# Performance work log

Hardware: AMD Instinct MI355X
Metric: run time of the kernel (lower is better)

The kernel has to match this reference:

```python
import jax, jax.numpy as jnp
from jax import lax
import numpy as np

B, TE, TD, C, H, L, V, BLOCK = 2, 1024, 1024, 512, 8, 4, 32000, 1024
HD = C // H  # 64


def setup_inputs() -> dict:
    key = jax.random.key(0)
    ks = iter(jax.random.split(key, 64))
    def w(*shape):
        return jax.random.normal(next(ks), shape, jnp.float32) * 0.02
    d = {}
    d["enc_inp"] = jax.random.randint(next(ks), (B, TE), 0, V, dtype=jnp.int32)
    d["dec_inp"] = jax.random.randint(next(ks), (B, TD), 0, V, dtype=jnp.int32)
    d["enc_inp_mask"] = jnp.ones((B, TE), jnp.int32)
    d["tok_emb"] = w(V, C)
    d["pos_emb"] = w(BLOCK, C)
    for p in ["e", "d_sa", "d_ca"]:
        d[p + "_wq"] = w(L, H, C, HD)
        d[p + "_wk"] = w(L, H, C, HD)
        d[p + "_wv"] = w(L, H, C, HD)
        d[p + "_wo"] = w(L, C, C)
        d[p + "_bo"] = jnp.zeros((L, C), jnp.float32)
    for n in ["e_ln1", "e_ln2", "d_ln1", "d_ln2", "d_ln3"]:
        d[n + "_g"] = jnp.ones((L, C), jnp.float32)
        d[n + "_b"] = jnp.zeros((L, C), jnp.float32)
    for p in ["e", "d"]:
        d[p + "_w1"] = w(L, C, 4 * C)
        d[p + "_b1"] = jnp.zeros((L, 4 * C), jnp.float32)
        d[p + "_w2"] = w(L, 4 * C, C)
        d[p + "_b2"] = jnp.zeros((L, C), jnp.float32)
    d["out_w"] = w(C, V)
    d["out_b"] = jnp.zeros((V,), jnp.float32)
    return d


def _ln(x, g, b):
    m = jnp.mean(x, -1, keepdims=True)
    v = jnp.mean((x - m) ** 2, -1, keepdims=True)
    return (x - m) / jnp.sqrt(v + 1e-5) * g + b


def _mha(x, kv, wq, wk, wv, wo, bo, mask, causal):
    # x: [B,T,C], kv: [B,S,C], wq/wk/wv: [H,C,HD]
    q = jnp.einsum('btc,hcd->bhtd', x, wq)
    k = jnp.einsum('bsc,hcd->bhsd', kv, wk)
    v = jnp.einsum('bsc,hcd->bhsd', kv, wv)
    s = jnp.einsum('bhtd,bhsd->bhts', q, k) * (HD ** -0.5)
    if causal:
        T, S = s.shape[-2], s.shape[-1]
        s = jnp.where(jnp.tril(jnp.ones((T, S), bool)), s, -jnp.inf)
    if mask is not None:
        s = jnp.where(mask[:, None, None, :] != 0, s, -jnp.inf)
    a = jax.nn.softmax(s, axis=-1)
    o = jnp.einsum('bhts,bhsd->bthd', a, v).reshape(x.shape[0], x.shape[1], -1)
    return o @ wo + bo


def reference(enc_inp, dec_inp, enc_inp_mask, tok_emb, pos_emb,
              e_wq, e_wk, e_wv, e_wo, e_bo,
              d_sa_wq, d_sa_wk, d_sa_wv, d_sa_wo, d_sa_bo,
              d_ca_wq, d_ca_wk, d_ca_wv, d_ca_wo, d_ca_bo,
              e_ln1_g, e_ln1_b, e_ln2_g, e_ln2_b,
              d_ln1_g, d_ln1_b, d_ln2_g, d_ln2_b, d_ln3_g, d_ln3_b,
              e_w1, e_b1, e_w2, e_b2, d_w1, d_b1, d_w2, d_b2,
              out_w, out_b):
    enc = tok_emb[enc_inp] + pos_emb[:enc_inp.shape[1]]
    dec = tok_emb[dec_inp] + pos_emb[:dec_inp.shape[1]]

    def enc_step(x, p):
        ln1g, ln1b, wq, wk, wv, wo, bo, ln2g, ln2b, w1, b1, w2, b2 = p
        h = _ln(x, ln1g, ln1b)
        x = x + _mha(h, h, wq, wk, wv, wo, bo, enc_inp_mask, False)
        h = _ln(x, ln2g, ln2b)
        x = x + jnp.maximum(h @ w1 + b1, 0.0) @ w2 + b2
        return x, None

    enc_out, _ = lax.scan(enc_step, enc, (e_ln1_g, e_ln1_b, e_wq, e_wk, e_wv, e_wo, e_bo,
                                          e_ln2_g, e_ln2_b, e_w1, e_b1, e_w2, e_b2))

    def dec_step(x, p):
        (ln1g, ln1b, sawq, sawk, sawv, sawo, sabo,
         ln2g, ln2b, cawq, cawk, cawv, cawo, cabo,
         ln3g, ln3b, w1, b1, w2, b2) = p
        h = _ln(x, ln1g, ln1b)
        x = x + _mha(h, h, sawq, sawk, sawv, sawo, sabo, None, True)
        # torch code applies the same cross-attn LayerNorm to both x and encoder_output
        hq = _ln(x, ln2g, ln2b)
        hk = _ln(enc_out, ln2g, ln2b)
        x = x + _mha(hq, hk, cawq, cawk, cawv, cawo, cabo, enc_inp_mask, False)
        h = _ln(x, ln3g, ln3b)
        x = x + jnp.maximum(h @ w1 + b1, 0.0) @ w2 + b2
        return x, None

    dec_out, _ = lax.scan(dec_step, dec, (d_ln1_g, d_ln1_b, d_sa_wq, d_sa_wk, d_sa_wv, d_sa_wo, d_sa_bo,
                                          d_ln2_g, d_ln2_b, d_ca_wq, d_ca_wk, d_ca_wv, d_ca_wo, d_ca_bo,
                                          d_ln3_g, d_ln3_b, d_w1, d_b1, d_w2, d_b2))

    logits = dec_out @ out_w + out_b  # [B, T_dec, V]
    return logits
```

## Files before the change

### kernel.cpp

```cpp
#include <hip/hip_runtime.h>
#include <hip/hip_bf16.h>
#include <math.h>

#define Cdim 512
#define Hn   8
#define HDim 64
#define Ld   4
#define Tn   1024
#define Bn   2
#define NTOK 2048
#define FF   2048
#define Vn   32000

typedef __bf16 bf16_t;
typedef __bf16 bf16x8 __attribute__((ext_vector_type(8)));
typedef __bf16 bf16x4 __attribute__((ext_vector_type(4)));
typedef float  f32x4  __attribute__((ext_vector_type(4)));

__device__ __forceinline__ void ln_wave(const float* __restrict__ xr,
    const float* __restrict__ g, const float* __restrict__ bb,
    bf16_t* __restrict__ yr, int lane)
{
    f32x4 a = *(const f32x4*)&xr[lane * 8];
    f32x4 c = *(const f32x4*)&xr[lane * 8 + 4];
    float s = a[0] + a[1] + a[2] + a[3] + c[0] + c[1] + c[2] + c[3];
    #pragma unroll
    for (int o = 1; o < 64; o <<= 1) s += __shfl_xor(s, o, 64);
    float mean = s * (1.f / Cdim);
    float d[8], qv = 0.f;
    #pragma unroll
    for (int k = 0; k < 4; k++) { d[k] = a[k] - mean; d[4 + k] = c[k] - mean; }
    #pragma unroll
    for (int k = 0; k < 8; k++) qv += d[k] * d[k];
    #pragma unroll
    for (int o = 1; o < 64; o <<= 1) qv += __shfl_xor(qv, o, 64);
    float inv = rsqrtf(qv * (1.f / Cdim) + 1e-5f);
    f32x4 g0 = *(const f32x4*)&g[lane * 8],  g1 = *(const f32x4*)&g[lane * 8 + 4];
    f32x4 b0 = *(const f32x4*)&bb[lane * 8], b1 = *(const f32x4*)&bb[lane * 8 + 4];
    bf16x8 o;
    #pragma unroll
    for (int k = 0; k < 4; k++) {
        o[k]     = (bf16_t)(d[k]     * inv * g0[k] + b0[k]);
        o[4 + k] = (bf16_t)(d[4 + k] * inv * g1[k] + b1[k]);
    }
    *(bf16x8*)&yr[lane * 8] = o;
}

__global__ __launch_bounds__(256) void ln_k(const float* __restrict__ x,
    const float* __restrict__ g, const float* __restrict__ bb, bf16_t* __restrict__ y)
{
    int wid = threadIdx.x >> 6, lane = threadIdx.x & 63;
    int row = blockIdx.x * 4 + wid;
    ln_wave(x + (long)row * Cdim, g, bb, y + (long)row * Cdim, lane);
}

__global__ __launch_bounds__(256) void ln2_k(const float* __restrict__ x1,
    const float* __restrict__ x2, const float* __restrict__ g,
    const float* __restrict__ bb, bf16_t* __restrict__ y1, bf16_t* __restrict__ y2)
{
    int wid = threadIdx.x >> 6, lane = threadIdx.x & 63;
    int row = blockIdx.x * 4 + wid;
    const float* x = (row < NTOK) ? x1 : x2;
    bf16_t*      y = (row < NTOK) ? y1 : y2;
    int r = row & (NTOK - 1);
    ln_wave(x + (long)r * Cdim, g, bb, y + (long)r * Cdim, lane);
}

__global__ __launch_bounds__(256) void embed_ln_k(const int* __restrict__ inp,
    const float* __restrict__ tok, const float* __restrict__ pos,
    const float* __restrict__ g, const float* __restrict__ bb,
    float* __restrict__ x, bf16_t* __restrict__ y)
{
    int wid = threadIdx.x >> 6, lane = threadIdx.x & 63;
    int bt = blockIdx.x * 4 + wid;
    int t = bt & (Tn - 1);
    long toff = (long)inp[bt] * Cdim;
    f32x4 a = *(const f32x4*)&tok[toff + lane * 8];
    f32x4 c = *(const f32x4*)&tok[toff + lane * 8 + 4];
    f32x4 pa = *(const f32x4*)&pos[(long)t * Cdim + lane * 8];
    f32x4 pc = *(const f32x4*)&pos[(long)t * Cdim + lane * 8 + 4];
    a += pa; c += pc;
    float* xr = x + (long)bt * Cdim;
    *(f32x4*)&xr[lane * 8] = a;
    *(f32x4*)&xr[lane * 8 + 4] = c;
    float s = a[0] + a[1] + a[2] + a[3] + c[0] + c[1] + c[2] + c[3];
    #pragma unroll
    for (int o = 1; o < 64; o <<= 1) s += __shfl_xor(s, o, 64);
    float mean = s * (1.f / Cdim);
    float d[8], qv = 0.f;
    #pragma unroll
    for (int k = 0; k < 4; k++) { d[k] = a[k] - mean; d[4 + k] = c[k] - mean; }
    #pragma unroll
    for (int k = 0; k < 8; k++) qv += d[k] * d[k];
    #pragma unroll
    for (int o = 1; o < 64; o <<= 1) qv += __shfl_xor(qv, o, 64);
    float inv = rsqrtf(qv * (1.f / Cdim) + 1e-5f);
    f32x4 g0 = *(const f32x4*)&g[lane * 8],  g1 = *(const f32x4*)&g[lane * 8 + 4];
    f32x4 b0 = *(const f32x4*)&bb[lane * 8], b1 = *(const f32x4*)&bb[lane * 8 + 4];
    bf16x8 o;
    #pragma unroll
    for (int k = 0; k < 4; k++) {
        o[k]     = (bf16_t)(d[k]     * inv * g0[k] + b0[k]);
        o[4 + k] = (bf16_t)(d[4 + k] * inv * g1[k] + b1[k]);
    }
    *(bf16x8*)&y[(long)bt * Cdim + lane * 8] = o;
}

struct Ptr3 { const float* p[3]; };
__global__ __launch_bounds__(256) void tcvt_b_k(Ptr3 srcs, bf16_t* __restrict__ dst,
    int R, int Cc, int lps, long dstStride)
{
    int z = blockIdx.z; int s = z / lps, l = z - s * lps;
    const float* in = srcs.p[s] + (long)l * R * Cc;
    bf16_t* op = dst + (long)z * dstStride;
    __shared__ float t[64][65];
    int r0 = blockIdx.y * 64, c0 = blockIdx.x * 64;
    int tx = threadIdx.x & 63, ty = threadIdx.x >> 6;
    #pragma unroll
    for (int i = 0; i < 16; i++)
        t[ty + i * 4][tx] = in[(long)(r0 + ty + i * 4) * Cc + c0 + tx];
    __syncthreads();
    #pragma unroll
    for (int i = 0; i < 16; i++) {
        int cc = ty + i * 4;
        op[(long)(c0 + cc) * R + r0 + tx] = (bf16_t)t[tx][cc];
    }
}

struct QkvSrc { const float* p[9]; };
__global__ __launch_bounds__(256) void tcvt_qkv_k(QkvSrc srcs, bf16_t* __restrict__ outp)
{
    int z = blockIdx.z;
    int si = z >> 5, zb = (z >> 3) & 3, zh = z & 7;
    int set = si / 3, part = si - set * 3;
    const float* in = srcs.p[si] + (long)zb * (Hn * Cdim * HDim) + (long)zh * (Cdim * HDim);
    bf16_t* op = outp + ((long)set * Ld + zb) * (1536L * Cdim)
                      + (long)part * 512 * Cdim + (long)zh * 64 * Cdim;
    __shared__ float t[64][65];
    int r0 = blockIdx.y * 64;
    int tx = threadIdx.x & 63, ty = threadIdx.x >> 6;
    #pragma unroll
    for (int i = 0; i < 16; i++)
        t[ty + i * 4][tx] = in[(long)(r0 + ty + i * 4) * HDim + tx];
    __syncthreads();
    #pragma unroll
    for (int i = 0; i < 16; i++) {
        int cc = ty + i * 4;
        op[(long)cc * Cdim + r0 + tx] = (bf16_t)t[tx][cc];
    }
}

template<int BM, int BN, int BK, bool BIAS, bool RELU, bool RES, bool OBF,
         bool VOUT, int SWZM, bool XOUT, bool COAL>
__global__ __launch_bounds__(256) void mgemm_k(
    const bf16_t* __restrict__ A, const bf16_t* __restrict__ A2, int aSplit,
    const bf16_t* __restrict__ Bt, const float* __restrict__ bias,
    const float* __restrict__ res, void* __restrict__ Cout,
    bf16_t* __restrict__ xout, bf16_t* __restrict__ vtout, int vSplit,
    int K, int lda, int ldb, int ldc)
{
    constexpr int MR = BM / 32;
    constexpr int NR = BN / 32;
    constexpr int KK = BK / 32;
    constexpr int LPR = BK / 8;
    __shared__ bf16_t As0[BM * BK];
    __shared__ bf16_t As1[BM * BK];
    __shared__ bf16_t Bs0[BN * BK];
    __shared__ bf16_t Bs1[BN * BK];
    __shared__ float cws[COAL ? 4 * 16 * 36 : 1];

    int tid = threadIdx.x;
    int wv = tid >> 6, lane = tid & 63;
    int bm, bn;
    if constexpr (SWZM > 0) {
        int lin = blockIdx.y * gridDim.x + blockIdx.x;
        int tot = gridDim.x * gridDim.y;
        int chunk = tot >> 3;
        int e = (lin & 7) * chunk + (lin >> 3);
        bm = (e % SWZM) * BM;
        bn = (e / SWZM) * BN;
    } else {
        bm = blockIdx.y * BM; bn = blockIdx.x * BN;
    }
    const bf16_t* Ab = (bn < aSplit) ? A : A2;
    int wr = wv >> 1, wc = wv & 1;

    f32x4 acc[MR][NR];
    #pragma unroll
    for (int i = 0; i < MR; i++)
        #pragma unroll
        for (int j = 0; j < NR; j++)
            acc[i][j] = (f32x4){0.f, 0.f, 0.f, 0.f};

    constexpr int RPW = 512 / BK;
    constexpr int RPP = 2048 / BK;
    const int sr  = lane / LPR;
    const int sc8 = ((lane % LPR) ^ (sr & (LPR - 1))) * 8;
    const int r16 = lane & 15, g4 = lane >> 4;

    auto stage = [&](int k0, bf16_t (&Asb)[BM * BK], bf16_t (&Bsb)[BN * BK]) {
        #pragma unroll
        for (int p = 0; p < BM * BK / 2048; p++) {
            int rb = p * RPP + wv * RPW;
            const bf16_t* g = Ab + (long)(bm + rb + sr) * lda + (k0 + sc8);
            __builtin_amdgcn_global_load_lds(
                (const __attribute__((address_space(1))) void*)g,
                (__attribute__((address_space(3))) void*)&Asb[rb * BK],
                16, 0, 0);
        }
        #pragma unroll
        for (int p = 0; p < BN * BK / 2048; p++) {
            int rb = p * RPP + wv * RPW;
            const bf16_t* g = Bt + (long)(bn + rb + sr) * ldb + (k0 + sc8);
            __builtin_amdgcn_global_load_lds(
                (const __attribute__((address_space(1))) void*)g,
                (__attribute__((address_space(3))) void*)&Bsb[rb * BK],
                16, 0, 0);
        }
    };
    auto compute = [&](bf16_t (&Asb)[BM * BK], bf16_t (&Bsb)[BN * BK]) {
        #pragma unroll
        for (int kk = 0; kk < KK; kk++) {
            bf16x8 bkk[NR];
            #pragma unroll
            for (int j = 0; j < NR; j++) {
                int row = wc * (BN / 2) + j * 16 + r16;
                bkk[j] = *(const bf16x8*)&Bsb[row * BK + (((kk * 4 + g4) ^ (row & (LPR - 1))) * 8)];
            }
            #pragma unroll
            for (int i = 0; i < MR; i++) {
                int row = wr * (BM / 2) + i * 16 + r16;
                bf16x8 a = *(const bf16x8*)&Asb[row * BK + (((kk * 4 + g4) ^ (row & (LPR - 1))) * 8)];
                #pragma unroll
                for (int j = 0; j < NR; j++)
                    acc[i][j] = __builtin_amdgcn_mfma_f32_16x16x32_bf16(a, bkk[j], acc[i][j], 0, 0, 0);
            }
        }
    };

    int nIt = K / BK;
    stage(0, As0, Bs0);
    for (int it = 0; it < nIt; it += 2) {
        __syncthreads();
        if (it + 1 < nIt) stage((it + 1) * BK, As1, Bs1);
        compute(As0, Bs0);
        __syncthreads();
        if (it + 2 < nIt) stage((it + 2) * BK, As0, Bs0);
        if (it + 1 < nIt) compute(As1, Bs1);
    }

    if constexpr (COAL) {
        #pragma unroll
        for (int i = 0; i < MR; i++) {
            int gr0 = bm + wr * (BM / 2) + i * 16;
            #pragma unroll
            for (int hh = 0; hh < NR / 2; hh++) {
                #pragma unroll
                for (int jj = 0; jj < 2; jj++) {
                    int j = hh * 2 + jj;
                    int gc = bn + wc * (BN / 2) + j * 16 + r16;
                    float bv = BIAS ? bias[gc] : 0.f;
                    #pragma unroll
                    for (int q = 0; q < 4; q++) {
                        float v = acc[i][j][q];
                        if (BIAS) v += bv;
                        if (RELU) v = fmaxf(v, 0.f);
                        cws[(wv * 16 + g4 * 4 + q) * 36 + jj * 16 + r16] = v;
                    }
                }
                int gcb = bn + wc * (BN / 2) + hh * 32;
                if constexpr (OBF) {
                    int row = lane >> 2, c8 = (lane & 3) * 8;
                    f32x4 v0 = *(f32x4*)&cws[(wv * 16 + row) * 36 + c8];
                    f32x4 v1 = *(f32x4*)&cws[(wv * 16 + row) * 36 + c8 + 4];
                    long oidx = (long)(gr0 + row) * ldc + gcb + c8;
                    bf16x8 o;
                    #pragma unroll
                    for (int k = 0; k < 4; k++) { o[k] = (bf16_t)v0[k]; o[4 + k] = (bf16_t)v1[k]; }
                    *(bf16x8*)&((bf16_t*)Cout)[oidx] = o;
                } else {
                    #pragma unroll
                    for (int ps = 0; ps < 2; ps++) {
                        int row = (lane >> 3) + 8 * ps, c4 = (lane & 7) * 4;
                        f32x4 v = *(f32x4*)&cws[(wv * 16 + row) * 36 + c4];
                        long oidx = (long)(gr0 + row) * ldc + gcb + c4;
                        if (RES) v += *(const f32x4*)&res[oidx];
                        *(f32x4*)&((float*)Cout)[oidx] = v;
                        if (XOUT) {
                            bf16x4 o;
                            #pragma unroll
                            for (int k = 0; k < 4; k++) o[k] = (bf16_t)v[k];
                            *(bf16x4*)&xout[oidx] = o;
                        }
                    }
                }
            }
        }
    } else {
        #pragma unroll
        for (int i = 0; i < MR; i++) {
            #pragma unroll
            for (int j = 0; j < NR; j++) {
                int gr = bm + wr * (BM / 2) + i * 16 + g4 * 4;
                int gc = bn + wc * (BN / 2) + j * 16 + r16;
                float bv = BIAS ? bias[gc] : 0.f;
                #pragma unroll
                for (int q = 0; q < 4; q++) {
                    float v = acc[i][j][q];
                    if (BIAS) v += bv;
                    if (RELU) v = fmaxf(v, 0.f);
                    if (VOUT && gc >= vSplit) {
                        int row = gr + q;
                        int b = row >> 10, t = row & (Tn - 1);
                        vtout[((long)b * 512 + (gc - vSplit)) * Tn + t] = (bf16_t)v;
                    } else {
                        long oidx = (long)(gr + q) * ldc + gc;
                        if (RES)  v += res[oidx];
                        if (OBF) ((bf16_t*)Cout)[oidx] = (bf16_t)v;
                        else     ((float*) Cout)[oidx] = v;
                        if (XOUT) xout[oidx] = (bf16_t)v;
                    }
                }
            }
        }
    }
}

template<bool CAUSAL, bool HASMASK>
__global__ __launch_bounds__(512, 2) void flash_k(
    const bf16_t* __restrict__ qkv, const bf16_t* __restrict__ vt,
    const int* __restrict__ mask, bf16_t* __restrict__ ao)
{
    __shared__ bf16_t Kl[2][2][64][72];
    __shared__ bf16_t Vl[2][2][64][72];
    __shared__ bf16_t Pl[8][16][72];

    int qt = blockIdx.x, bh = blockIdx.y;
    int b = bh >> 3, h = bh & 7;
    int tid = threadIdx.x, wv = tid >> 6, lane = tid & 63;
    int wg = wv >> 2, wq4 = wv & 3;
    int r16 = lane & 15, g4 = lane >> 4;
    int gtid = tid & 255;

    const bf16_t* qb = qkv + ((long)(b * Tn + qt * 64 + wq4 * 16 + r16)) * 1536 + h * 64;
    bf16x8 aq0 = *(const bf16x8*)&qb[g4 * 8];
    bf16x8 aq1 = *(const bf16x8*)&qb[32 + g4 * 8];

    f32x4 acc[4];
    #pragma unroll
    for (int j = 0; j < 4; j++) acc[j] = (f32x4){0.f, 0.f, 0.f, 0.f};
    float m_[4], l_[4];
    #pragma unroll
    for (int q = 0; q < 4; q++) { m_[q] = -1e30f; l_[q] = 0.f; }

    int lastT = CAUSAL ? qt : (Tn / 64 - 1);
    int niter = CAUSAL ? (qt / 2 + 1) : (Tn / 128);
    int krow = gtid >> 3, kcol = (gtid & 7) * 8;

    bf16x8 kr[2], vr[2];
    int mv = 0;
    {
        int t0 = wg;
        if (t0 <= lastT) {
            int s0 = t0 * 64;
            #pragma unroll
            for (int i = 0; i < 2; i++)
                kr[i] = *(const bf16x8*)&qkv[((long)(b * Tn + s0 + krow + i * 32)) * 1536 + 512 + h * 64 + kcol];
            #pragma unroll
            for (int i = 0; i < 2; i++)
                vr[i] = *(const bf16x8*)&vt[((long)(bh * 64 + krow + i * 32)) * Tn + s0 + kcol];
            if (HASMASK) mv = mask[b * Tn + s0 + lane];
        }
    }

    for (int it = 0; it < niter; it++) {
        int cur = it & 1;
        int t = 2 * it + wg;
        bool active = t <= lastT;
        if (active) {
            #pragma unroll
            for (int i = 0; i < 2; i++) *(bf16x8*)&Kl[cur][wg][krow + i * 32][kcol] = kr[i];
            #pragma unroll
            for (int i = 0; i < 2; i++) *(bf16x8*)&Vl[cur][wg][krow + i * 32][kcol] = vr[i];
        }
        int mv_use = mv;
        __syncthreads();
        int tn = t + 2;
        if (it + 1 < niter && tn <= lastT) {
            int sn = tn * 64;
            #pragma unroll
            for (int i = 0; i < 2; i++)
                kr[i] = *(const bf16x8*)&qkv[((long)(b * Tn + sn + krow + i * 32)) * 1536 + 512 + h * 64 + kcol];
            #pragma unroll
            for (int i = 0; i < 2; i++)
                vr[i] = *(const bf16x8*)&vt[((long)(bh * 64 + krow + i * 32)) * Tn + sn + kcol];
            if (HASMASK) mv = mask[b * Tn + sn + lane];
        }
        if (!active) continue;

        f32x4 scv[4];
        __builtin_amdgcn_s_setprio(1);
        #pragma unroll
        for (int j = 0; j < 4; j++) {
            scv[j] = (f32x4){0.f, 0.f, 0.f, 0.f};
            bf16x8 bk0 = *(const bf16x8*)&Kl[cur][wg][j * 16 + r16][g4 * 8];
            bf16x8 bk1 = *(const bf16x8*)&Kl[cur][wg][j * 16 + r16][32 + g4 * 8];
            scv[j] = __builtin_amdgcn_mfma_f32_16x16x32_bf16(aq0, bk0, scv[j], 0, 0, 0);
            scv[j] = __builtin_amdgcn_mfma_f32_16x16x32_bf16(aq1, bk1, scv[j], 0, 0, 0);
        }
        __builtin_amdgcn_s_setprio(0);

        bool diag = CAUSAL && (t == qt);
        #pragma unroll
        for (int j = 0; j < 4; j++) {
            int col = j * 16 + r16;
            int mm = 1;
            if (HASMASK) mm = __shfl(mv_use, col, 64);
            #pragma unroll
            for (int q = 0; q < 4; q++) {
                float v = scv[j][q] * 0.125f;
                if (diag && col > wq4 * 16 + g4 * 4 + q) v = -1e30f;
                if (HASMASK && mm == 0) v = -1e30f;
                scv[j][q] = v;
            }
        }

        float pmax[4];
        #pragma unroll
        for (int q = 0; q < 4; q++) {
            float v = fmaxf(fmaxf(scv[0][q], scv[1][q]), fmaxf(scv[2][q], scv[3][q]));
            v = fmaxf(v, __shfl_xor(v, 1, 64));
            v = fmaxf(v, __shfl_xor(v, 2, 64));
            v = fmaxf(v, __shfl_xor(v, 4, 64));
            v = fmaxf(v, __shfl_xor(v, 8, 64));
            pmax[q] = v;
        }
        bool skip = __all(pmax[0] <= m_[0] + 8.f && pmax[1] <= m_[1] + 8.f &&
                          pmax[2] <= m_[2] + 8.f && pmax[3] <= m_[3] + 8.f);
        if (!skip) {
            #pragma unroll
            for (int q = 0; q < 4; q++) {
                float mnew = fmaxf(m_[q], pmax[q]);
                float rf = __expf(m_[q] - mnew);
                l_[q] *= rf;
                #pragma unroll
                for (int j = 0; j < 4; j++) acc[j][q] *= rf;
                m_[q] = mnew;
            }
        }
        #pragma unroll
        for (int q = 0; q < 4; q++) {
            float rs = 0.f;
            #pragma unroll
            for (int j = 0; j < 4; j++) {
                float pv = __expf(scv[j][q] - m_[q]);
                scv[j][q] = pv;
                rs += pv;
            }
            rs += __shfl_xor(rs, 1, 64);
            rs += __shfl_xor(rs, 2, 64);
            rs += __shfl_xor(rs, 4, 64);
            rs += __shfl_xor(rs, 8, 64);
            l_[q] += rs;
        }

        #pragma unroll
        for (int j = 0; j < 4; j++)
            #pragma unroll
            for (int q = 0; q < 4; q++)
                Pl[wv][g4 * 4 + q][j * 16 + r16] = (bf16_t)scv[j][q];
        asm volatile("s_waitcnt lgkmcnt(0)" ::: "memory");
        __builtin_amdgcn_sched_barrier(0);

        __builtin_amdgcn_s_setprio(1);
        #pragma unroll
        for (int c = 0; c < 2; c++) {
            bf16x8 pa = *(const bf16x8*)&Pl[wv][r16][c * 32 + g4 * 8];
            #pragma unroll
            for (int j = 0; j < 4; j++) {
                bf16x8 bv = *(const bf16x8*)&Vl[cur][wg][j * 16 + r16][c * 32 + g4 * 8];
                acc[j] = __builtin_amdgcn_mfma_f32_16x16x32_bf16(pa, bv, acc[j], 0, 0, 0);
            }
        }
        __builtin_amdgcn_s_setprio(0);
    }

    float* accS = (float*)&Kl[0][0][0][0];
    float* mlS  = accS + 64 * 64;
    __syncthreads();
    if (wg == 1) {
        #pragma unroll
        for (int j = 0; j < 4; j++)
            #pragma unroll
            for (int q = 0; q < 4; q++)
                accS[(wq4 * 16 + g4 * 4 + q) * 64 + j * 16 + r16] = acc[j][q];
        if (r16 == 0)
            #pragma unroll
            for (int q = 0; q < 4; q++) {
                mlS[(wq4 * 16 + g4 * 4 + q) * 2 + 0] = m_[q];
                mlS[(wq4 * 16 + g4 * 4 + q) * 2 + 1] = l_[q];
            }
    }
    __syncthreads();
    if (wg == 0) {
        bf16_t* aob = ao + ((long)(b * Tn + qt * 64 + wq4 * 16 + g4 * 4)) * Cdim + h * 64;
        #pragma unroll
        for (int q = 0; q < 4; q++) {
            int row = wq4 * 16 + g4 * 4 + q;
            float mB = mlS[row * 2], lB = mlS[row * 2 + 1];
            float mS = fmaxf(m_[q], mB);
            float fA = __expf(m_[q] - mS), fB = __expf(mB - mS);
            float lS = l_[q] * fA + lB * fB;
            float inv = 1.f / lS;
            #pragma unroll
            for (int j = 0; j < 4; j++) {
                float o = (acc[j][q] * fA + accS[row * 64 + j * 16 + r16] * fB) * inv;
                aob[(long)q * Cdim + j * 16 + r16] = (bf16_t)o;
            }
        }
    }
}

static void run_attn(hipStream_t stream, const bf16_t* hq, const bf16_t* hkv,
    const bf16_t* wqkv, const float* bo, const bf16_t* wo_t,
    float* xres, const int* mask, bool causal,
    bf16_t* qkv, bf16_t* vt, bf16_t* ao)
{
    dim3 blk(256);
    mgemm_k<64,128,64,false,false,false,true,true,0,false,false><<<dim3(12, 32, 1), blk, 0, stream>>>(
        hq, hkv, 512, wqkv, nullptr, nullptr, qkv, nullptr, vt, 1024,
        Cdim, Cdim, Cdim, 1536);
    if (causal)
        flash_k<true,false><<<dim3(Tn / 64, Bn * Hn), dim3(512), 0, stream>>>(qkv, vt, nullptr, ao);
    else
        flash_k<false,true><<<dim3(Tn / 64, Bn * Hn), dim3(512), 0, stream>>>(qkv, vt, mask, ao);
    mgemm_k<64,64,64,true,false,true,false,false,0,false,true><<<dim3(8, 32, 1), blk, 0, stream>>>(
        ao, ao, 1 << 30, wo_t, bo, xres, xres, nullptr, nullptr, 1 << 30,
        Cdim, Cdim, Cdim, Cdim);
}

extern "C" void kernel_launch(void* const* d_in, const int* in_sizes, int n_in,
                              void* d_out, int out_size, void* d_ws, size_t ws_size,
                              hipStream_t stream)
{
    (void)in_sizes; (void)n_in; (void)out_size; (void)ws_size;
    const int*   enc_inp  = (const int*)d_in[0];
    const int*   dec_inp  = (const int*)d_in[1];
    const int*   enc_mask = (const int*)d_in[2];
    const float* tok_emb  = (const float*)d_in[3];
    const float* pos_emb  = (const float*)d_in[4];
    const float* e_wq  = (const float*)d_in[5];
    const float* e_wk  = (const float*)d_in[6];
    const float* e_wv  = (const float*)d_in[7];
    const float* e_wo  = (const float*)d_in[8];
    const float* e_bo  = (const float*)d_in[9];
    const float* dsa_wq = (const float*)d_in[10];
    const float* dsa_wk = (const float*)d_in[11];
    const float* dsa_wv = (const float*)d_in[12];
    const float* dsa_wo = (const float*)d_in[13];
    const float* dsa_bo = (const float*)d_in[14];
    const float* dca_wq = (const float*)d_in[15];
    const float* dca_wk = (const float*)d_in[16];
    const float* dca_wv = (const float*)d_in[17];
    const float* dca_wo = (const float*)d_in[18];
    const float* dca_bo = (const float*)d_in[19];
    const float* e_ln1_g = (const float*)d_in[20];
    const float* e_ln1_b = (const float*)d_in[21];
    const float* e_ln2_g = (const float*)d_in[22];
    const float* e_ln2_b = (const float*)d_in[23];
    const float* d_ln1_g = (const float*)d_in[24];
    const float* d_ln1_b = (const float*)d_in[25];
    const float* d_ln2_g = (const float*)d_in[26];
    const float* d_ln2_b = (const float*)d_in[27];
    const float* d_ln3_g = (const float*)d_in[28];
    const float* d_ln3_b = (const float*)d_in[29];
    const float* e_w1 = (const float*)d_in[30];
    const float* e_b1 = (const float*)d_in[31];
    const float* e_w2 = (const float*)d_in[32];
    const float* e_b2 = (const float*)d_in[33];
    const float* d_w1 = (const float*)d_in[34];
    const float* d_b1 = (const float*)d_in[35];
    const float* d_w2 = (const float*)d_in[36];
    const float* d_b2 = (const float*)d_in[37];
    const float* out_w = (const float*)d_in[38];
    const float* out_b = (const float*)d_in[39];
    float* out = (float*)d_out;

    char* p = (char*)d_ws;
    auto takeB = [&](size_t bytes) { char* r = p; p += (bytes + 255) & ~(size_t)255; return r; };
    float*  x_enc = (float*)takeB(1048576ull * 4);
    float*  x_dec = (float*)takeB(1048576ull * 4);
    bf16_t* h     = (bf16_t*)takeB(1048576ull * 2);
    bf16_t* hk    = (bf16_t*)takeB(1048576ull * 2);
    bf16_t* qkv   = (bf16_t*)takeB(3145728ull * 2);
    bf16_t* vt    = (bf16_t*)takeB(1048576ull * 2);
    bf16_t* ao    = (bf16_t*)takeB(1048576ull * 2);
    bf16_t* xdb   = (bf16_t*)takeB(1048576ull * 2);
    bf16_t* mid   = (bf16_t*)takeB(4194304ull * 2);
    bf16_t* wqkv_t = (bf16_t*)takeB(12ull * 786432 * 2);
    bf16_t* wo_t   = (bf16_t*)takeB(12ull * 262144 * 2);
    bf16_t* w1_t   = (bf16_t*)takeB(8ull * 1048576 * 2);
    bf16_t* w2_t   = (bf16_t*)takeB(8ull * 1048576 * 2);
    bf16_t* outw_t = (bf16_t*)takeB(16384000ull * 2);

    dim3 blk(256);
    const long LQKV = 1536L * Cdim;

    QkvSrc qs;
    qs.p[0] = e_wq;   qs.p[1] = e_wk;   qs.p[2] = e_wv;
    qs.p[3] = dsa_wq; qs.p[4] = dsa_wk; qs.p[5] = dsa_wv;
    qs.p[6] = dca_wq; qs.p[7] = dca_wk; qs.p[8] = dca_wv;
    tcvt_qkv_k<<<dim3(1, 8, 288), blk, 0, stream>>>(qs, wqkv_t);
    Ptr3 pw;
    pw.p[0] = e_wo; pw.p[1] = dsa_wo; pw.p[2] = dca_wo;
    tcvt_b_k<<<dim3(8, 8, 12), blk, 0, stream>>>(pw, wo_t, Cdim, Cdim, 4, (long)Cdim * Cdim);
    pw.p[0] = e_w1; pw.p[1] = d_w1; pw.p[2] = nullptr;
    tcvt_b_k<<<dim3(32, 8, 8), blk, 0, stream>>>(pw, w1_t, Cdim, FF, 4, (long)Cdim * FF);
    pw.p[0] = e_w2; pw.p[1] = d_w2; pw.p[2] = nullptr;
    tcvt_b_k<<<dim3(8, 32, 8), blk, 0, stream>>>(pw, w2_t, FF, Cdim, 4, (long)FF * Cdim);
    pw.p[0] = out_w; pw.p[1] = nullptr; pw.p[2] = nullptr;
    tcvt_b_k<<<dim3(500, 8, 1), blk, 0, stream>>>(pw, outw_t, Cdim, Vn, 1, 0);

    embed_ln_k<<<NTOK / 4, blk, 0, stream>>>(enc_inp, tok_emb, pos_emb, e_ln1_g, e_ln1_b, x_enc, h);
    for (int l = 0; l < Ld; l++) {
        if (l) ln_k<<<NTOK / 4, blk, 0, stream>>>(x_enc, e_ln1_g + l * Cdim, e_ln1_b + l * Cdim, h);
        run_attn(stream, h, h,
                 wqkv_t + (long)l * LQKV, e_bo + l * Cdim, wo_t + (long)l * Cdim * Cdim,
                 x_enc, enc_mask, false, qkv, vt, ao);
        ln_k<<<NTOK / 4, blk, 0, stream>>>(x_enc, e_ln2_g + l * Cdim, e_ln2_b + l * Cdim, h);
        mgemm_k<128,128,64,true,true,false,true,false,0,false,true><<<dim3(16, 16, 1), blk, 0, stream>>>(
            h, h, 1 << 30, w1_t + (long)l * Cdim * FF, e_b1 + l * FF, nullptr, mid,
            nullptr, nullptr, 1 << 30, Cdim, Cdim, Cdim, FF);
        mgemm_k<64,64,64,true,false,true,false,false,0,false,true><<<dim3(8, 32, 1), blk, 0, stream>>>(
            mid, mid, 1 << 30, w2_t + (long)l * FF * Cdim, e_b2 + l * Cdim, x_enc, x_enc,
            nullptr, nullptr, 1 << 30, FF, FF, FF, Cdim);
    }

    embed_ln_k<<<NTOK / 4, blk, 0, stream>>>(dec_inp, tok_emb, pos_emb, d_ln1_g, d_ln1_b, x_dec, h);
    for (int l = 0; l < Ld; l++) {
        if (l) ln_k<<<NTOK / 4, blk, 0, stream>>>(x_dec, d_ln1_g + l * Cdim, d_ln1_b + l * Cdim, h);
        run_attn(stream, h, h,
                 wqkv_t + (long)(Ld + l) * LQKV, dsa_bo + l * Cdim,
                 wo_t + (long)(Ld + l) * Cdim * Cdim,
                 x_dec, nullptr, true, qkv, vt, ao);
        ln2_k<<<2 * NTOK / 4, blk, 0, stream>>>(x_dec, x_enc,
            d_ln2_g + l * Cdim, d_ln2_b + l * Cdim, h, hk);
        run_attn(stream, h, hk,
                 wqkv_t + (long)(2 * Ld + l) * LQKV, dca_bo + l * Cdim,
                 wo_t + (long)(2 * Ld + l) * Cdim * Cdim,
                 x_dec, enc_mask, false, qkv, vt, ao);
        ln_k<<<NTOK / 4, blk, 0, stream>>>(x_dec, d_ln3_g + l * Cdim, d_ln3_b + l * Cdim, h);
        mgemm_k<128,128,64,true,true,false,true,false,0,false,true><<<dim3(16, 16, 1), blk, 0, stream>>>(
            h, h, 1 << 30, w1_t + (long)(Ld + l) * Cdim * FF, d_b1 + l * FF, nullptr, mid,
            nullptr, nullptr, 1 << 30, Cdim, Cdim, Cdim, FF);
        if (l < Ld - 1)
            mgemm_k<64,64,64,true,false,true,false,false,0,false,true><<<dim3(8, 32, 1), blk, 0, stream>>>(
                mid, mid, 1 << 30, w2_t + (long)(Ld + l) * FF * Cdim, d_b2 + l * Cdim, x_dec, x_dec,
                nullptr, nullptr, 1 << 30, FF, FF, FF, Cdim);
        else
            mgemm_k<64,64,64,true,false,true,false,false,0,true,true><<<dim3(8, 32, 1), blk, 0, stream>>>(
                mid, mid, 1 << 30, w2_t + (long)(Ld + l) * FF * Cdim, d_b2 + l * Cdim, x_dec, x_dec,
                xdb, nullptr, 1 << 30, FF, FF, FF, Cdim);
    }

    mgemm_k<128,128,64,true,false,false,false,false,16,false,true><<<dim3(250, 16, 1), blk, 0, stream>>>(
        xdb, xdb, 1 << 30, outw_t, out_b, nullptr, out, nullptr, nullptr, 1 << 30,
        Cdim, Cdim, Cdim, Vn);
}
```

Before: 1.005 ms.

## Shrink flash-attention blocks to 32 query rows with 4 waves, single-buffered LDS

The flash attention kernel now handles 32 query rows per block with 256 threads (two KV groups of two waves each) instead of 64 rows with 512 threads. This doubles the grid and spreads the causal workload more evenly across CUs. The K/V shared tiles drop from double to single buffering, with a second barrier per iteration to keep reuse safe. The smaller LDS footprint and the new launch bounds allow more blocks per CU, at the cost of an extra sync per iteration and re-loading K/V for each half of the former query tile.

```diff
diff --git a/kernel.cpp b/kernel.cpp
--- a/kernel.cpp
+++ b/kernel.cpp
@@ -327,22 +327,21 @@
 }
 
 template<bool CAUSAL, bool HASMASK>
-__global__ __launch_bounds__(512, 2) void flash_k(
+__global__ __launch_bounds__(256, 3) void flash_k(
     const bf16_t* __restrict__ qkv, const bf16_t* __restrict__ vt,
     const int* __restrict__ mask, bf16_t* __restrict__ ao)
 {
-    __shared__ bf16_t Kl[2][2][64][72];
-    __shared__ bf16_t Vl[2][2][64][72];
-    __shared__ bf16_t Pl[8][16][72];
-
-    int qt = blockIdx.x, bh = blockIdx.y;
+    __shared__ bf16_t Kl[2][64][72];
+    __shared__ bf16_t Vl[2][64][72];
+    __shared__ bf16_t Pl[4][16][72];
+
+    int qx = blockIdx.x, bh = blockIdx.y;
     int b = bh >> 3, h = bh & 7;
     int tid = threadIdx.x, wv = tid >> 6, lane = tid & 63;
-    int wg = wv >> 2, wq4 = wv & 3;
+    int wg = wv >> 1, wq = wv & 1;
     int r16 = lane & 15, g4 = lane >> 4;
-    int gtid = tid & 255;
-
-    const bf16_t* qb = qkv + ((long)(b * Tn + qt * 64 + wq4 * 16 + r16)) * 1536 + h * 64;
+
+    const bf16_t* qb = qkv + ((long)(b * Tn + qx * 32 + wq * 16 + r16)) * 1536 + h * 64;
     bf16x8 aq0 = *(const bf16x8*)&qb[g4 * 8];
     bf16x8 aq1 = *(const bf16x8*)&qb[32 + g4 * 8];
 
@@ -353,35 +352,35 @@
     #pragma unroll
     for (int q = 0; q < 4; q++) { m_[q] = -1e30f; l_[q] = 0.f; }
 
-    int lastT = CAUSAL ? qt : (Tn / 64 - 1);
-    int niter = CAUSAL ? (qt / 2 + 1) : (Tn / 128);
-    int krow = gtid >> 3, kcol = (gtid & 7) * 8;
-
-    bf16x8 kr[2], vr[2];
+    int lastT = CAUSAL ? (qx >> 1) : (Tn / 64 - 1);
+    int niter = CAUSAL ? ((qx >> 2) + 1) : (Tn / 128);
+    int st = tid & 127;
+    int srow = st >> 3, scol = (st & 7) * 8;
+
+    bf16x8 kr[4], vr[4];
     int mv = 0;
     {
         int t0 = wg;
         if (t0 <= lastT) {
             int s0 = t0 * 64;
             #pragma unroll
-            for (int i = 0; i < 2; i++)
-                kr[i] = *(const bf16x8*)&qkv[((long)(b * Tn + s0 + krow + i * 32)) * 1536 + 512 + h * 64 + kcol];
-            #pragma unroll
-            for (int i = 0; i < 2; i++)
-                vr[i] = *(const bf16x8*)&vt[((long)(bh * 64 + krow + i * 32)) * Tn + s0 + kcol];
+            for (int i = 0; i < 4; i++)
+                kr[i] = *(const bf16x8*)&qkv[((long)(b * Tn + s0 + srow + i * 16)) * 1536 + 512 + h * 64 + scol];
+            #pragma unroll
+            for (int i = 0; i < 4; i++)
+                vr[i] = *(const bf16x8*)&vt[((long)(bh * 64 + srow + i * 16)) * Tn + s0 + scol];
             if (HASMASK) mv = mask[b * Tn + s0 + lane];
         }
     }
 
     for (int it = 0; it < niter; it++) {
-        int cur = it & 1;
         int t = 2 * it + wg;
         bool active = t <= lastT;
         if (active) {
             #pragma unroll
-            for (int i = 0; i < 2; i++) *(bf16x8*)&Kl[cur][wg][krow + i * 32][kcol] = kr[i];
-            #pragma unroll
-            for (int i = 0; i < 2; i++) *(bf16x8*)&Vl[cur][wg][krow + i * 32][kcol] = vr[i];
+            for (int i = 0; i < 4; i++) *(bf16x8*)&Kl[wg][srow + i * 16][scol] = kr[i];
+            #pragma unroll
+            for (int i = 0; i < 4; i++) *(bf16x8*)&Vl[wg][srow + i * 16][scol] = vr[i];
         }
         int mv_use = mv;
         __syncthreads();
@@ -389,124 +388,124 @@
         if (it + 1 < niter && tn <= lastT) {
             int sn = tn * 64;
             #pragma unroll
-            for (int i = 0; i < 2; i++)
-                kr[i] = *(const bf16x8*)&qkv[((long)(b * Tn + sn + krow + i * 32)) * 1536 + 512 + h * 64 + kcol];
-            #pragma unroll
-            for (int i = 0; i < 2; i++)
-                vr[i] = *(const bf16x8*)&vt[((long)(bh * 64 + krow + i * 32)) * Tn + sn + kcol];
+            for (int i = 0; i < 4; i++)
+                kr[i] = *(const bf16x8*)&qkv[((long)(b * Tn + sn + srow + i * 16)) * 1536 + 512 + h * 64 + scol];
+            #pragma unroll
+            for (int i = 0; i < 4; i++)
+                vr[i] = *(const bf16x8*)&vt[((long)(bh * 64 + srow + i * 16)) * Tn + sn + scol];
             if (HASMASK) mv = mask[b * Tn + sn + lane];
         }
-        if (!active) continue;
-
-        f32x4 scv[4];
-        __builtin_amdgcn_s_setprio(1);
-        #pragma unroll
-        for (int j = 0; j < 4; j++) {
-            scv[j] = (f32x4){0.f, 0.f, 0.f, 0.f};
-            bf16x8 bk0 = *(const bf16x8*)&Kl[cur][wg][j * 16 + r16][g4 * 8];
-            bf16x8 bk1 = *(const bf16x8*)&Kl[cur][wg][j * 16 + r16][32 + g4 * 8];
-            scv[j] = __builtin_amdgcn_mfma_f32_16x16x32_bf16(aq0, bk0, scv[j], 0, 0, 0);
-            scv[j] = __builtin_amdgcn_mfma_f32_16x16x32_bf16(aq1, bk1, scv[j], 0, 0, 0);
-        }
-        __builtin_amdgcn_s_setprio(0);
-
-        bool diag = CAUSAL && (t == qt);
-        #pragma unroll
-        for (int j = 0; j < 4; j++) {
-            int col = j * 16 + r16;
-            int mm = 1;
-            if (HASMASK) mm = __shfl(mv_use, col, 64);
+        if (active) {
+            f32x4 scv[4];
+            __builtin_amdgcn_s_setprio(1);
+            #pragma unroll
+            for (int j = 0; j < 4; j++) {
+                scv[j] = (f32x4){0.f, 0.f, 0.f, 0.f};
+                bf16x8 bk0 = *(const bf16x8*)&Kl[wg][j * 16 + r16][g4 * 8];
+                bf16x8 bk1 = *(const bf16x8*)&Kl[wg][j * 16 + r16][32 + g4 * 8];
+                scv[j] = __builtin_amdgcn_mfma_f32_16x16x32_bf16(aq0, bk0, scv[j], 0, 0, 0);
+                scv[j] = __builtin_amdgcn_mfma_f32_16x16x32_bf16(aq1, bk1, scv[j], 0, 0, 0);
+            }
+            __builtin_amdgcn_s_setprio(0);
+
+            bool diag = CAUSAL && (t == lastT);
+            #pragma unroll
+            for (int j = 0; j < 4; j++) {
+                int col = j * 16 + r16;
+                int mm = 1;
+                if (HASMASK) mm = __shfl(mv_use, col, 64);
+                #pragma unroll
+                for (int q = 0; q < 4; q++) {
+                    float v = scv[j][q] * 0.125f;
+                    if (diag && col > (qx & 1) * 32 + wq * 16 + g4 * 4 + q) v = -1e30f;
+                    if (HASMASK && mm == 0) v = -1e30f;
+                    scv[j][q] = v;
+                }
+            }
+
+            float pmax[4];
             #pragma unroll
             for (int q = 0; q < 4; q++) {
-                float v = scv[j][q] * 0.125f;
-                if (diag && col > wq4 * 16 + g4 * 4 + q) v = -1e30f;
-                if (HASMASK && mm == 0) v = -1e30f;
-                scv[j][q] = v;
-            }
-        }
-
-        float pmax[4];
-        #pragma unroll
-        for (int q = 0; q < 4; q++) {
-            float v = fmaxf(fmaxf(scv[0][q], scv[1][q]), fmaxf(scv[2][q], scv[3][q]));
-            v = fmaxf(v, __shfl_xor(v, 1, 64));
-            v = fmaxf(v, __shfl_xor(v, 2, 64));
-            v = fmaxf(v, __shfl_xor(v, 4, 64));
-            v = fmaxf(v, __shfl_xor(v, 8, 64));
-            pmax[q] = v;
-        }
-        bool skip = __all(pmax[0] <= m_[0] + 8.f && pmax[1] <= m_[1] + 8.f &&
-                          pmax[2] <= m_[2] + 8.f && pmax[3] <= m_[3] + 8.f);
-        if (!skip) {
+                float v = fmaxf(fmaxf(scv[0][q], scv[1][q]), fmaxf(scv[2][q], scv[3][q]));
+                v = fmaxf(v, __shfl_xor(v, 1, 64));
+                v = fmaxf(v, __shfl_xor(v, 2, 64));
+                v = fmaxf(v, __shfl_xor(v, 4, 64));
+                v = fmaxf(v, __shfl_xor(v, 8, 64));
+                pmax[q] = v;
+            }
+            bool skip = __all(pmax[0] <= m_[0] + 8.f && pmax[1] <= m_[1] + 8.f &&
+                              pmax[2] <= m_[2] + 8.f && pmax[3] <= m_[3] + 8.f);
+            if (!skip) {
+                #pragma unroll
+                for (int q = 0; q < 4; q++) {
+                    float mnew = fmaxf(m_[q], pmax[q]);
+                    float rf = __expf(m_[q] - mnew);
+                    l_[q] *= rf;
+                    #pragma unroll
+                    for (int j = 0; j < 4; j++) acc[j][q] *= rf;
+                    m_[q] = mnew;
+                }
+            }
             #pragma unroll
             for (int q = 0; q < 4; q++) {
-                float mnew = fmaxf(m_[q], pmax[q]);
-                float rf = __expf(m_[q] - mnew);
-                l_[q] *= rf;
-                #pragma unroll
-                for (int j = 0; j < 4; j++) acc[j][q] *= rf;
-                m_[q] = mnew;
-            }
-        }
-        #pragma unroll
-        for (int q = 0; q < 4; q++) {
-            float rs = 0.f;
-            #pragma unroll
-            for (int j = 0; j < 4; j++) {
-                float pv = __expf(scv[j][q] - m_[q]);
-                scv[j][q] = pv;
-                rs += pv;
-            }
-            rs += __shfl_xor(rs, 1, 64);
-            rs += __shfl_xor(rs, 2, 64);
-            rs += __shfl_xor(rs, 4, 64);
-            rs += __shfl_xor(rs, 8, 64);
-            l_[q] += rs;
-        }
-
+                float rs = 0.f;
+                #pragma unroll
+                for (int j = 0; j < 4; j++) {
+                    float pv = __expf(scv[j][q] - m_[q]);
+                    scv[j][q] = pv;
+                    rs += pv;
+                }
+                rs += __shfl_xor(rs, 1, 64);
+                rs += __shfl_xor(rs, 2, 64);
+                rs += __shfl_xor(rs, 4, 64);
+                rs += __shfl_xor(rs, 8, 64);
+                l_[q] += rs;
+            }
+
+            #pragma unroll
+            for (int j = 0; j < 4; j++)
+                #pragma unroll
+                for (int q = 0; q < 4; q++)
+                    Pl[wv][g4 * 4 + q][j * 16 + r16] = (bf16_t)scv[j][q];
+            asm volatile("s_waitcnt lgkmcnt(0)" ::: "memory");
+            __builtin_amdgcn_sched_barrier(0);
+
+            __builtin_amdgcn_s_setprio(1);
+            #pragma unroll
+            for (int c = 0; c < 2; c++) {
+                bf16x8 pa = *(const bf16x8*)&Pl[wv][r16][c * 32 + g4 * 8];
+                #pragma unroll
+                for (int j = 0; j < 4; j++) {
+                    bf16x8 bv = *(const bf16x8*)&Vl[wg][j * 16 + r16][c * 32 + g4 * 8];
+                    acc[j] = __builtin_amdgcn_mfma_f32_16x16x32_bf16(pa, bv, acc[j], 0, 0, 0);
+                }
+            }
+            __builtin_amdgcn_s_setprio(0);
+        }
+        __syncthreads();
+    }
+
+    float* accS = (float*)&Kl[0][0][0];
+    float* mlS  = accS + 32 * 64;
+    if (wg == 1) {
         #pragma unroll
         for (int j = 0; j < 4; j++)
             #pragma unroll
             for (int q = 0; q < 4; q++)
-                Pl[wv][g4 * 4 + q][j * 16 + r16] = (bf16_t)scv[j][q];
-        asm volatile("s_waitcnt lgkmcnt(0)" ::: "memory");
-        __builtin_amdgcn_sched_barrier(0);
-
-        __builtin_amdgcn_s_setprio(1);
-        #pragma unroll
-        for (int c = 0; c < 2; c++) {
-            bf16x8 pa = *(const bf16x8*)&Pl[wv][r16][c * 32 + g4 * 8];
-            #pragma unroll
-            for (int j = 0; j < 4; j++) {
-                bf16x8 bv = *(const bf16x8*)&Vl[cur][wg][j * 16 + r16][c * 32 + g4 * 8];
-                acc[j] = __builtin_amdgcn_mfma_f32_16x16x32_bf16(pa, bv, acc[j], 0, 0, 0);
-            }
-        }
-        __builtin_amdgcn_s_setprio(0);
-    }
-
-    float* accS = (float*)&Kl[0][0][0][0];
-    float* mlS  = accS + 64 * 64;
-    __syncthreads();
-    if (wg == 1) {
-        #pragma unroll
-        for (int j = 0; j < 4; j++)
-            #pragma unroll
-            for (int q = 0; q < 4; q++)
-                accS[(wq4 * 16 + g4 * 4 + q) * 64 + j * 16 + r16] = acc[j][q];
+                accS[(wq * 16 + g4 * 4 + q) * 64 + j * 16 + r16] = acc[j][q];
         if (r16 == 0)
             #pragma unroll
             for (int q = 0; q < 4; q++) {
-                mlS[(wq4 * 16 + g4 * 4 + q) * 2 + 0] = m_[q];
-                mlS[(wq4 * 16 + g4 * 4 + q) * 2 + 1] = l_[q];
+                mlS[(wq * 16 + g4 * 4 + q) * 2 + 0] = m_[q];
+                mlS[(wq * 16 + g4 * 4 + q) * 2 + 1] = l_[q];
             }
     }
     __syncthreads();
     if (wg == 0) {
-        bf16_t* aob = ao + ((long)(b * Tn + qt * 64 + wq4 * 16 + g4 * 4)) * Cdim + h * 64;
+        bf16_t* aob = ao + ((long)(b * Tn + qx * 32 + wq * 16 + g4 * 4)) * Cdim + h * 64;
         #pragma unroll
         for (int q = 0; q < 4; q++) {
-            int row = wq4 * 16 + g4 * 4 + q;
+            int row = wq * 16 + g4 * 4 + q;
             float mB = mlS[row * 2], lB = mlS[row * 2 + 1];
             float mS = fmaxf(m_[q], mB);
             float fA = __expf(m_[q] - mS), fB = __expf(mB - mS);
@@ -531,9 +530,9 @@
         hq, hkv, 512, wqkv, nullptr, nullptr, qkv, nullptr, vt, 1024,
         Cdim, Cdim, Cdim, 1536);
     if (causal)
-        flash_k<true,false><<<dim3(Tn / 64, Bn * Hn), dim3(512), 0, stream>>>(qkv, vt, nullptr, ao);
+        flash_k<true,false><<<dim3(Tn / 32, Bn * Hn), dim3(256), 0, stream>>>(qkv, vt, nullptr, ao);
     else
-        flash_k<false,true><<<dim3(Tn / 64, Bn * Hn), dim3(512), 0, stream>>>(qkv, vt, mask, ao);
+        flash_k<false,true><<<dim3(Tn / 32, Bn * Hn), dim3(256), 0, stream>>>(qkv, vt, mask, ao);
     mgemm_k<64,64,64,true,false,true,false,false,0,false,true><<<dim3(8, 32, 1), blk, 0, stream>>>(
         ao, ao, 1 << 30, wo_t, bo, xres, xres, nullptr, nullptr, 1 << 30,
         Cdim, Cdim, Cdim, Cdim);
```

Measured after the change: 1.030 ms. 1.02x slower.
